# Optimization experiments

Hardware: AMD Instinct MI355X
Metric: run time of the kernel (lower is better)

## Reference

```python
import jax, jax.numpy as jnp
import numpy as np

N = 500000      # nodes
F_IN = 10       # node_features
HID = 32        # DCRNN hidden
OUT = 2         # out_features
E = 8000000     # edges (unused in math since K=1, kept for interface fidelity)


def setup_inputs() -> dict:
    key = jax.random.key(0)
    ks = jax.random.split(key, 12)
    d_in = F_IN + HID  # 42: DConv input is cat([X, H])
    s = 0.1
    return {
        "x": jax.random.normal(ks[0], (N, F_IN), dtype=jnp.float32),
        "edge_index": jax.random.randint(ks[1], (2, E), 0, N, dtype=jnp.int64),
        "edge_weight": jax.random.uniform(ks[2], (E,), dtype=jnp.float32),
        "h": jax.random.normal(ks[3], (N, HID), dtype=jnp.float32),
        # DConv weights: torch shape (2, K=1, in, out); K dim squeezed -> (2, in, out)
        "W_z": jax.random.normal(ks[4], (2, d_in, HID), dtype=jnp.float32) * s,
        "b_z": jnp.zeros((HID,), dtype=jnp.float32),
        "W_r": jax.random.normal(ks[5], (2, d_in, HID), dtype=jnp.float32) * s,
        "b_r": jnp.zeros((HID,), dtype=jnp.float32),
        "W_h": jax.random.normal(ks[6], (2, d_in, HID), dtype=jnp.float32) * s,
        "b_h": jnp.zeros((HID,), dtype=jnp.float32),
        "W_lin": jax.random.normal(ks[7], (OUT, HID), dtype=jnp.float32) * s,
        "b_lin": jnp.zeros((OUT,), dtype=jnp.float32),
    }


def _dconv_k1(xh, W, b):
    # K=1 DConv: out/in diffusion weights collapse to a single dense transform
    return xh @ (W[0] + W[1]) + b


def reference(x, edge_index, edge_weight, h, W_z, b_z, W_r, b_r, W_h, b_h, W_lin, b_lin):
    # DCRNN GRU step (edge_index/edge_weight unused because K=1)
    xh = jnp.concatenate([x, h], axis=1)                  # [N, F_IN+HID]
    z = jax.nn.sigmoid(_dconv_k1(xh, W_z, b_z))           # update gate
    r = jax.nn.sigmoid(_dconv_k1(xh, W_r, b_r))           # reset gate
    xrh = jnp.concatenate([x, r * h], axis=1)
    h_tilde = jnp.tanh(_dconv_k1(xrh, W_h, b_h))
    h_new = z * h + (1.0 - z) * h_tilde                   # [N, HID]
    out = jnp.maximum(h_new, 0.0) @ W_lin.T + b_lin       # ReLU + Linear head, [N, OUT]
    return (out, h_new)
```

## Files before the change

### kernel.cpp

```cpp
#include <hip/hip_runtime.h>
#include <stdint.h>

static constexpr int N_NODES = 500000;

typedef __attribute__((ext_vector_type(8))) short short8;
typedef __attribute__((ext_vector_type(4))) float f32x4;


__device__ __forceinline__ float bfdec(uint32_t b){
  union{uint32_t u; float f;} c; c.u = b << 16; return c.f;
}
__device__ __forceinline__ uint32_t bfrne(float f){
  union{float f; uint32_t u;} c; c.f = f;
  return (c.u + 0x7fffu + ((c.u >> 16) & 1u)) >> 16;
}
__device__ __forceinline__ uint32_t pack2(float a, float b){
  return bfrne(a) | (bfrne(b) << 16);
}
__device__ __forceinline__ float sigmoid_fast(float x){
  float e = __expf(-x);
  return __builtin_amdgcn_rcpf(1.0f + e);
}
__device__ __forceinline__ float tanh_fast(float x){
  float e = __expf(2.0f * x);
  return 1.0f - 2.0f * __builtin_amdgcn_rcpf(e + 1.0f);
}

__device__ bool detect_f32_words(const uint32_t* w, int K){
  float m = 0.0f;
  for (int i = 0; i < K; i++) m = fmaxf(m, fabsf(bfdec(w[i] & 0xffffu)));
  return !(m < 1e6f);
}
__device__ __forceinline__ float wload(const void* p, int idx, bool f32w){
  if (f32w) return ((const float*)p)[idx];
  return bfdec(((const uint16_t*)p)[idx]);
}

__global__ void prep_kernel(const void* __restrict__ Wz,
                            const void* __restrict__ bz,
                            const void* __restrict__ Wr,
                            const void* __restrict__ br,
                            const void* __restrict__ Wh,
                            const void* __restrict__ bh,
                            const void* __restrict__ Wl,
                            const void* __restrict__ bl,
                            const uint32_t* __restrict__ xg,
                            const uint32_t* __restrict__ hg,
                            float* __restrict__ ws)
{
  const bool f32w = detect_f32_words((const uint32_t*)Wz, 64);
  uint16_t* wsh = (uint16_t*)ws;
  float*    wsf = ws;
  int i = blockIdx.x * 256 + threadIdx.x;
  if (i < 4608) {
    float v = 0.0f;
    if (i < 3072) {
      int col = i / 48, k = i - col * 48;
      if (k < 42) {
        const void* Wp = (col < 32) ? Wz : Wr;
        int j = (col < 32) ? col : col - 32;
        int src = k * 32 + j;
        v = wload(Wp, src, f32w) + wload(Wp, 1344 + src, f32w);
      }
    } else {
      int b2 = i - 3072;
      int col = b2 / 48, k = b2 - col * 48;
      if (k < 42) {
        int src = k * 32 + col;
        v = wload(Wh, src, f32w) + wload(Wh, 1344 + src, f32w);
      }
    }
    wsh[i] = (uint16_t)bfrne(v);
  } else if (i < 4608 + 162) {
    int r = i - 4608;
    if      (r < 32)  wsf[2304 + r]        = wload(bz, r,     f32w);
    else if (r < 64)  wsf[2336 + (r-32)]   = wload(br, r-32,  f32w);
    else if (r < 96)  wsf[2368 + (r-64)]   = wload(bh, r-64,  f32w);
    else if (r < 160) wsf[2400 + (r-96)]   = wload(Wl, r-96,  f32w);
    else              wsf[2464 + (r-160)]  = wload(bl, r-160, f32w);
  } else if (i == 4800) {
    wsf[2466] = detect_f32_words(xg, 256) ? 1.0f : 0.0f;
  } else if (i == 4801) {
    wsf[2467] = detect_f32_words(hg, 256) ? 1.0f : 0.0f;
  }
}

__global__ __launch_bounds__(256, 4) void dcrnn_kernel(
    const uint32_t* __restrict__ xg,
    const uint32_t* __restrict__ hg,
    const float*    __restrict__ ws,
    float* __restrict__ out0,
    float* __restrict__ outh)
{
  __shared__ __align__(16) uint16_t w_u16[4608];
  __shared__ __align__(16) uint16_t xh_u16[256 * 48];

  const int t  = threadIdx.x;
  const int nd = blockIdx.x * 256 + t;
  const bool valid = nd < N_NODES;
  const float* wsf = ws;
  const bool x_f32 = wsf[2466] != 0.0f;
  const bool h_f32 = wsf[2467] != 0.0f;

  const uint4* wsq = (const uint4*)ws;
  for (int i = t; i < 576; i += 256) ((uint4*)w_u16)[i] = wsq[i];

  uint32_t rw[24];
  #pragma unroll
  for (int i = 0; i < 24; i++) rw[i] = 0u;
  if (valid) {
    if (x_f32) {
      const float2* xr = (const float2*)((const float*)xg + (size_t)nd * 10);
      #pragma unroll
      for (int i = 0; i < 5; i++){ float2 v = xr[i]; rw[i] = pack2(v.x, v.y); }
    } else {
      const uint32_t* xr = xg + (size_t)nd * 5;
      #pragma unroll
      for (int i = 0; i < 5; i++) rw[i] = xr[i];
    }
    if (h_f32) {
      const float4* hr = (const float4*)((const float*)hg + (size_t)nd * 32);
      #pragma unroll
      for (int i = 0; i < 8; i++){
        float4 v = hr[i];
        rw[5 + 2*i]     = pack2(v.x, v.y);
        rw[5 + 2*i + 1] = pack2(v.z, v.w);
      }
    } else {
      const uint4* hr = (const uint4*)(hg + (size_t)nd * 16);
      #pragma unroll
      for (int i = 0; i < 4; i++){
        uint4 v = hr[i];
        rw[5 + 4*i]     = v.x; rw[5 + 4*i + 1] = v.y;
        rw[5 + 4*i + 2] = v.z; rw[5 + 4*i + 3] = v.w;
      }
    }
  }
  {
    uint4* dst = (uint4*)(xh_u16 + t * 48);
    #pragma unroll
    for (int c = 0; c < 6; c++)
      dst[c] = make_uint4(rw[4*c], rw[4*c+1], rw[4*c+2], rw[4*c+3]);
  }
  __syncthreads();

  const int l = t & 63, w = t >> 6;
  const int lo16 = l & 15, g = l >> 4;
  uint16_t* xwm = xh_u16 + (w * 64) * 48;

  const float bzc0 = wsf[2304 + lo16], bzc1 = wsf[2320 + lo16];
  const float brc0 = wsf[2336 + lo16], brc1 = wsf[2352 + lo16];
  const float bhc0 = wsf[2368 + lo16], bhc1 = wsf[2384 + lo16];

  const short8 zero8 = {0,0,0,0,0,0,0,0};

  #pragma unroll
  for (int mt = 0; mt < 4; mt++){
    const uint16_t* arow = xwm + (mt*16 + lo16) * 48;
    short8 a0 = *(const short8*)(arow + g*8);
    short8 a1 = zero8;
    if (g < 2) a1 = *(const short8*)(arow + 32 + g*8);

    f32x4 accZ0 = {bzc0,bzc0,bzc0,bzc0};
    f32x4 accZ1 = {bzc1,bzc1,bzc1,bzc1};
    f32x4 accR0 = {brc0,brc0,brc0,brc0};
    f32x4 accR1 = {brc1,brc1,brc1,brc1};
    #pragma unroll
    for (int nt = 0; nt < 4; nt++){
      const uint16_t* brow = w_u16 + (nt*16 + lo16) * 48;
      short8 b0 = *(const short8*)(brow + g*8);
      short8 b1 = zero8;
      if (g < 2) b1 = *(const short8*)(brow + 32 + g*8);
      f32x4 acc = (nt==0)?accZ0:(nt==1)?accZ1:(nt==2)?accR0:accR1;
      acc = __builtin_amdgcn_mfma_f32_16x16x32_bf16(a0, b0, acc, 0, 0, 0);
      acc = __builtin_amdgcn_mfma_f32_16x16x32_bf16(a1, b1, acc, 0, 0, 0);
      if (nt==0) accZ0 = acc; else if (nt==1) accZ1 = acc;
      else if (nt==2) accR0 = acc; else accR1 = acc;
    }

    f32x4 hs0, hs1;
    #pragma unroll
    for (int q = 0; q < 4; q++){
      int row = mt*16 + g*4 + q;
      uint16_t* p0 = xwm + row*48 + 10 + lo16;
      uint16_t* p1 = xwm + row*48 + 26 + lo16;
      float h0 = bfdec(*p0), h1 = bfdec(*p1);
      float r0 = sigmoid_fast(accR0[q]);
      float r1 = sigmoid_fast(accR1[q]);
      *p0 = (uint16_t)bfrne(r0 * h0);
      *p1 = (uint16_t)bfrne(r1 * h1);
      hs0[q] = h0; hs1[q] = h1;
    }
    asm volatile("s_waitcnt lgkmcnt(0)" ::: "memory");

    f32x4 accH0 = {bhc0,bhc0,bhc0,bhc0};
    f32x4 accH1 = {bhc1,bhc1,bhc1,bhc1};
    short8 c0 = *(const short8*)(arow + g*8);
    short8 c1 = zero8;
    if (g < 2) c1 = *(const short8*)(arow + 32 + g*8);
    #pragma unroll
    for (int nt = 0; nt < 2; nt++){
      const uint16_t* brow = w_u16 + 3072 + (nt*16 + lo16) * 48;
      short8 b0 = *(const short8*)(brow + g*8);
      short8 b1 = zero8;
      if (g < 2) b1 = *(const short8*)(brow + 32 + g*8);
      f32x4 acc = (nt==0) ? accH0 : accH1;
      acc = __builtin_amdgcn_mfma_f32_16x16x32_bf16(c0, b0, acc, 0, 0, 0);
      acc = __builtin_amdgcn_mfma_f32_16x16x32_bf16(c1, b1, acc, 0, 0, 0);
      if (nt==0) accH0 = acc; else accH1 = acc;
    }

    #pragma unroll
    for (int q = 0; q < 4; q++){
      int row  = mt*16 + g*4 + q;
      int node = blockIdx.x*256 + w*64 + row;
      float z0 = sigmoid_fast(accZ0[q]);
      float z1 = sigmoid_fast(accZ1[q]);
      float t0 = tanh_fast(accH0[q]);
      float t1 = tanh_fast(accH1[q]);
      float hn0 = fmaf(z0, hs0[q] - t0, t0);
      float hn1 = fmaf(z1, hs1[q] - t1, t1);
      if (node < N_NODES){
        outh[(size_t)node*32 + lo16]      = hn0;
        outh[(size_t)node*32 + 16 + lo16] = hn1;
      }
      *(xwm + row*48 + 10 + lo16) = (uint16_t)bfrne(fmaxf(hn0, 0.0f));
      *(xwm + row*48 + 26 + lo16) = (uint16_t)bfrne(fmaxf(hn1, 0.0f));
    }
  }

  asm volatile("s_waitcnt lgkmcnt(0)" ::: "memory");
  if (valid){
    float o0 = wsf[2464], o1 = wsf[2465];
    const uint16_t* hr = xh_u16 + t*48 + 10;
    #pragma unroll
    for (int c = 0; c < 32; c++){
      float v = bfdec(hr[c]);
      o0 = fmaf(v, wsf[2400 + c], o0);
      o1 = fmaf(v, wsf[2432 + c], o1);
    }
    ((float2*)out0)[nd] = make_float2(o0, o1);
  }
}

extern "C" void kernel_launch(void* const* d_in, const int* in_sizes, int n_in,
                              void* d_out, int out_size, void* d_ws, size_t ws_size,
                              hipStream_t stream) {
  const uint32_t* x = (const uint32_t*)d_in[0];
  const uint32_t* h = (const uint32_t*)d_in[3];

  float* ws = (float*)d_ws;

  prep_kernel<<<19, 256, 0, stream>>>(d_in[4], d_in[5], d_in[6], d_in[7],
                                      d_in[8], d_in[9], d_in[10], d_in[11],
                                      x, h, ws);

  float* outf = (float*)d_out;
  float* out0 = outf;
  float* outh = outf + (size_t)2 * N_NODES;
  dcrnn_kernel<<<(N_NODES + 255) / 256, 256, 0, stream>>>(
      x, h, ws, out0, outh);
}
```

Before: 245.1 us.

## Pad LDS rows, hoist weight fragments to registers, compute output head with MFMA

Pads the LDS row stride from 48 to 56 halfwords to cut bank conflicts on both the weight and activation tiles. Loads the Z/R/H weight fragments into registers once per wave instead of re-reading them from LDS on every row tile. Replaces the per-thread 32-term scalar dot product for the linear head with one bf16 MFMA per tile, writing ReLU(h_new) over the first 32 columns of each row. This adds register pressure and changes the head's weights to bf16 precision.

```diff
diff --git a/kernel.cpp b/kernel.cpp
--- a/kernel.cpp
+++ b/kernel.cpp
@@ -2,6 +2,7 @@
 #include <stdint.h>
 
 static constexpr int N_NODES = 500000;
+static constexpr int STR     = 56;
 
 typedef __attribute__((ext_vector_type(8))) short short8;
 typedef __attribute__((ext_vector_type(4))) float f32x4;
@@ -52,10 +53,10 @@
   uint16_t* wsh = (uint16_t*)ws;
   float*    wsf = ws;
   int i = blockIdx.x * 256 + threadIdx.x;
-  if (i < 4608) {
+  if (i < 5376) {
     float v = 0.0f;
-    if (i < 3072) {
-      int col = i / 48, k = i - col * 48;
+    if (i < 3584) {
+      int col = i / STR, k = i - col * STR;
       if (k < 42) {
         const void* Wp = (col < 32) ? Wz : Wr;
         int j = (col < 32) ? col : col - 32;
@@ -63,25 +64,27 @@
         v = wload(Wp, src, f32w) + wload(Wp, 1344 + src, f32w);
       }
     } else {
-      int b2 = i - 3072;
-      int col = b2 / 48, k = b2 - col * 48;
+      int t2 = i - 3584;
+      int col = t2 / STR, k = t2 - col * STR;
       if (k < 42) {
         int src = k * 32 + col;
         v = wload(Wh, src, f32w) + wload(Wh, 1344 + src, f32w);
       }
     }
     wsh[i] = (uint16_t)bfrne(v);
-  } else if (i < 4608 + 162) {
-    int r = i - 4608;
-    if      (r < 32)  wsf[2304 + r]        = wload(bz, r,     f32w);
-    else if (r < 64)  wsf[2336 + (r-32)]   = wload(br, r-32,  f32w);
-    else if (r < 96)  wsf[2368 + (r-64)]   = wload(bh, r-64,  f32w);
-    else if (r < 160) wsf[2400 + (r-96)]   = wload(Wl, r-96,  f32w);
-    else              wsf[2464 + (r-160)]  = wload(bl, r-160, f32w);
-  } else if (i == 4800) {
-    wsf[2466] = detect_f32_words(xg, 256) ? 1.0f : 0.0f;
-  } else if (i == 4801) {
-    wsf[2467] = detect_f32_words(hg, 256) ? 1.0f : 0.0f;
+  } else if (i < 5440) {
+    int r = i - 5376;
+    wsh[i] = (uint16_t)bfrne(wload(Wl, r, f32w));
+  } else if (i < 5538) {
+    int r = i - 5440;
+    if      (r < 32) wsf[2720 + r]      = wload(bz, r,     f32w);
+    else if (r < 64) wsf[2752 + (r-32)] = wload(br, r-32,  f32w);
+    else if (r < 96) wsf[2784 + (r-64)] = wload(bh, r-64,  f32w);
+    else             wsf[2816 + (r-96)] = wload(bl, r-96,  f32w);
+  } else if (i == 5568) {
+    wsf[2818] = detect_f32_words(xg, 256) ? 1.0f : 0.0f;
+  } else if (i == 5569) {
+    wsf[2819] = detect_f32_words(hg, 256) ? 1.0f : 0.0f;
   }
 }
 
@@ -92,18 +95,18 @@
     float* __restrict__ out0,
     float* __restrict__ outh)
 {
-  __shared__ __align__(16) uint16_t w_u16[4608];
-  __shared__ __align__(16) uint16_t xh_u16[256 * 48];
+  __shared__ __align__(16) uint16_t w_u16[96 * STR];
+  __shared__ __align__(16) uint16_t xh_u16[256 * STR];
 
   const int t  = threadIdx.x;
   const int nd = blockIdx.x * 256 + t;
   const bool valid = nd < N_NODES;
   const float* wsf = ws;
-  const bool x_f32 = wsf[2466] != 0.0f;
-  const bool h_f32 = wsf[2467] != 0.0f;
+  const bool x_f32 = wsf[2818] != 0.0f;
+  const bool h_f32 = wsf[2819] != 0.0f;
 
   const uint4* wsq = (const uint4*)ws;
-  for (int i = t; i < 576; i += 256) ((uint4*)w_u16)[i] = wsq[i];
+  for (int i = t; i < 672; i += 256) ((uint4*)w_u16)[i] = wsq[i];
 
   uint32_t rw[24];
   #pragma unroll
@@ -137,7 +140,7 @@
     }
   }
   {
-    uint4* dst = (uint4*)(xh_u16 + t * 48);
+    uint4* dst = (uint4*)(xh_u16 + t * STR);
     #pragma unroll
     for (int c = 0; c < 6; c++)
       dst[c] = make_uint4(rw[4*c], rw[4*c+1], rw[4*c+2], rw[4*c+3]);
@@ -146,17 +149,37 @@
 
   const int l = t & 63, w = t >> 6;
   const int lo16 = l & 15, g = l >> 4;
-  uint16_t* xwm = xh_u16 + (w * 64) * 48;
-
-  const float bzc0 = wsf[2304 + lo16], bzc1 = wsf[2320 + lo16];
-  const float brc0 = wsf[2336 + lo16], brc1 = wsf[2352 + lo16];
-  const float bhc0 = wsf[2368 + lo16], bhc1 = wsf[2384 + lo16];
+  uint16_t* xwm = xh_u16 + (w * 64) * STR;
+
+  const float bzc0 = wsf[2720 + lo16], bzc1 = wsf[2736 + lo16];
+  const float brc0 = wsf[2752 + lo16], brc1 = wsf[2768 + lo16];
+  const float bhc0 = wsf[2784 + lo16], bhc1 = wsf[2800 + lo16];
+  const float blc  = (lo16 < 2) ? wsf[2816 + lo16] : 0.0f;
 
   const short8 zero8 = {0,0,0,0,0,0,0,0};
 
+  short8 bzr_lo[4], bzr_hi[4];
+  #pragma unroll
+  for (int nt = 0; nt < 4; nt++){
+    const uint16_t* brow = w_u16 + (nt*16 + lo16) * STR;
+    bzr_lo[nt] = *(const short8*)(brow + g*8);
+    bzr_hi[nt] = zero8;
+    if (g < 2) bzr_hi[nt] = *(const short8*)(brow + 32 + g*8);
+  }
+  short8 bh_lo[2], bh_hi[2];
+  #pragma unroll
+  for (int nt = 0; nt < 2; nt++){
+    const uint16_t* brow = w_u16 + 3584 + (nt*16 + lo16) * STR;
+    bh_lo[nt] = *(const short8*)(brow + g*8);
+    bh_hi[nt] = zero8;
+    if (g < 2) bh_hi[nt] = *(const short8*)(brow + 32 + g*8);
+  }
+  short8 bO = zero8;
+  if (lo16 < 2) bO = *(const short8*)((const uint16_t*)ws + 5376 + lo16*32 + g*8);
+
   #pragma unroll
   for (int mt = 0; mt < 4; mt++){
-    const uint16_t* arow = xwm + (mt*16 + lo16) * 48;
+    const uint16_t* arow = xwm + (mt*16 + lo16) * STR;
     short8 a0 = *(const short8*)(arow + g*8);
     short8 a1 = zero8;
     if (g < 2) a1 = *(const short8*)(arow + 32 + g*8);
@@ -165,25 +188,21 @@
     f32x4 accZ1 = {bzc1,bzc1,bzc1,bzc1};
     f32x4 accR0 = {brc0,brc0,brc0,brc0};
     f32x4 accR1 = {brc1,brc1,brc1,brc1};
-    #pragma unroll
-    for (int nt = 0; nt < 4; nt++){
-      const uint16_t* brow = w_u16 + (nt*16 + lo16) * 48;
-      short8 b0 = *(const short8*)(brow + g*8);
-      short8 b1 = zero8;
-      if (g < 2) b1 = *(const short8*)(brow + 32 + g*8);
-      f32x4 acc = (nt==0)?accZ0:(nt==1)?accZ1:(nt==2)?accR0:accR1;
-      acc = __builtin_amdgcn_mfma_f32_16x16x32_bf16(a0, b0, acc, 0, 0, 0);
-      acc = __builtin_amdgcn_mfma_f32_16x16x32_bf16(a1, b1, acc, 0, 0, 0);
-      if (nt==0) accZ0 = acc; else if (nt==1) accZ1 = acc;
-      else if (nt==2) accR0 = acc; else accR1 = acc;
-    }
+    accZ0 = __builtin_amdgcn_mfma_f32_16x16x32_bf16(a0, bzr_lo[0], accZ0, 0,0,0);
+    accZ0 = __builtin_amdgcn_mfma_f32_16x16x32_bf16(a1, bzr_hi[0], accZ0, 0,0,0);
+    accZ1 = __builtin_amdgcn_mfma_f32_16x16x32_bf16(a0, bzr_lo[1], accZ1, 0,0,0);
+    accZ1 = __builtin_amdgcn_mfma_f32_16x16x32_bf16(a1, bzr_hi[1], accZ1, 0,0,0);
+    accR0 = __builtin_amdgcn_mfma_f32_16x16x32_bf16(a0, bzr_lo[2], accR0, 0,0,0);
+    accR0 = __builtin_amdgcn_mfma_f32_16x16x32_bf16(a1, bzr_hi[2], accR0, 0,0,0);
+    accR1 = __builtin_amdgcn_mfma_f32_16x16x32_bf16(a0, bzr_lo[3], accR1, 0,0,0);
+    accR1 = __builtin_amdgcn_mfma_f32_16x16x32_bf16(a1, bzr_hi[3], accR1, 0,0,0);
 
     f32x4 hs0, hs1;
     #pragma unroll
     for (int q = 0; q < 4; q++){
       int row = mt*16 + g*4 + q;
-      uint16_t* p0 = xwm + row*48 + 10 + lo16;
-      uint16_t* p1 = xwm + row*48 + 26 + lo16;
+      uint16_t* p0 = xwm + row*STR + 10 + lo16;
+      uint16_t* p1 = xwm + row*STR + 26 + lo16;
       float h0 = bfdec(*p0), h1 = bfdec(*p1);
       float r0 = sigmoid_fast(accR0[q]);
       float r1 = sigmoid_fast(accR1[q]);
@@ -198,17 +217,10 @@
     short8 c0 = *(const short8*)(arow + g*8);
     short8 c1 = zero8;
     if (g < 2) c1 = *(const short8*)(arow + 32 + g*8);
-    #pragma unroll
-    for (int nt = 0; nt < 2; nt++){
-      const uint16_t* brow = w_u16 + 3072 + (nt*16 + lo16) * 48;
-      short8 b0 = *(const short8*)(brow + g*8);
-      short8 b1 = zero8;
-      if (g < 2) b1 = *(const short8*)(brow + 32 + g*8);
-      f32x4 acc = (nt==0) ? accH0 : accH1;
-      acc = __builtin_amdgcn_mfma_f32_16x16x32_bf16(c0, b0, acc, 0, 0, 0);
-      acc = __builtin_amdgcn_mfma_f32_16x16x32_bf16(c1, b1, acc, 0, 0, 0);
-      if (nt==0) accH0 = acc; else accH1 = acc;
-    }
+    accH0 = __builtin_amdgcn_mfma_f32_16x16x32_bf16(c0, bh_lo[0], accH0, 0,0,0);
+    accH0 = __builtin_amdgcn_mfma_f32_16x16x32_bf16(c1, bh_hi[0], accH0, 0,0,0);
+    accH1 = __builtin_amdgcn_mfma_f32_16x16x32_bf16(c0, bh_lo[1], accH1, 0,0,0);
+    accH1 = __builtin_amdgcn_mfma_f32_16x16x32_bf16(c1, bh_hi[1], accH1, 0,0,0);
 
     #pragma unroll
     for (int q = 0; q < 4; q++){
@@ -224,22 +236,20 @@
         outh[(size_t)node*32 + lo16]      = hn0;
         outh[(size_t)node*32 + 16 + lo16] = hn1;
       }
-      *(xwm + row*48 + 10 + lo16) = (uint16_t)bfrne(fmaxf(hn0, 0.0f));
-      *(xwm + row*48 + 26 + lo16) = (uint16_t)bfrne(fmaxf(hn1, 0.0f));
-    }
-  }
-
-  asm volatile("s_waitcnt lgkmcnt(0)" ::: "memory");
-  if (valid){
-    float o0 = wsf[2464], o1 = wsf[2465];
-    const uint16_t* hr = xh_u16 + t*48 + 10;
-    #pragma unroll
-    for (int c = 0; c < 32; c++){
-      float v = bfdec(hr[c]);
-      o0 = fmaf(v, wsf[2400 + c], o0);
-      o1 = fmaf(v, wsf[2432 + c], o1);
-    }
-    ((float2*)out0)[nd] = make_float2(o0, o1);
+      *(xwm + row*STR + lo16)      = (uint16_t)bfrne(fmaxf(hn0, 0.0f));
+      *(xwm + row*STR + 16 + lo16) = (uint16_t)bfrne(fmaxf(hn1, 0.0f));
+    }
+    asm volatile("s_waitcnt lgkmcnt(0)" ::: "memory");
+
+    short8 aO = *(const short8*)(arow + g*8);
+    f32x4 accO = {blc, blc, blc, blc};
+    accO = __builtin_amdgcn_mfma_f32_16x16x32_bf16(aO, bO, accO, 0,0,0);
+    #pragma unroll
+    for (int q = 0; q < 4; q++){
+      int node = blockIdx.x*256 + w*64 + mt*16 + g*4 + q;
+      if (lo16 < 2 && node < N_NODES)
+        out0[(size_t)node*2 + lo16] = accO[q];
+    }
   }
 }
 
@@ -251,7 +261,7 @@
 
   float* ws = (float*)d_ws;
 
-  prep_kernel<<<19, 256, 0, stream>>>(d_in[4], d_in[5], d_in[6], d_in[7],
+  prep_kernel<<<22, 256, 0, stream>>>(d_in[4], d_in[5], d_in[6], d_in[7],
                                       d_in[8], d_in[9], d_in[10], d_in[11],
                                       x, h, ws);
 
```

Result: no change. 248.6 us (+1.4%).
